# Performance work log

Measured on AMD Instinct MI355X. Metric: run time of the kernel, lower is better.

The kernel has to match this reference:

```python
import jax, jax.numpy as jnp
import numpy as np

EPS = 1e-5

def mean_std_norm(x):
    # instance norm without affine: per-(B,C) mean/std over spatial dims
    mean = jnp.mean(x, axis=(2, 3), keepdims=True)
    var = jnp.var(x, axis=(2, 3), keepdims=True)
    return (x - mean) / jnp.sqrt(var + EPS)

def conv1x1(x, w, b):
    # x: [B,C,H,W], w: [O,C], b: [O]
    return jnp.einsum('oc,bchw->bohw', w, x) + b[None, :, None, None]

def setup_inputs() -> dict:
    key = jax.random.key(0)
    ks = jax.random.split(key, 9)
    C = 512
    s = 1.0 / np.sqrt(C)
    inp = {
        'content_feat': jax.random.normal(ks[0], (4, C, 64, 64), dtype=jnp.float32),
        'f_w': jax.random.normal(ks[1], (C, C), dtype=jnp.float32) * s,
        'f_b': jnp.zeros((C,), dtype=jnp.float32),
        'g_w': jax.random.normal(ks[2], (C, C), dtype=jnp.float32) * s,
        'g_b': jnp.zeros((C,), dtype=jnp.float32),
        'h_w': jax.random.normal(ks[3], (C, C), dtype=jnp.float32) * s,
        'h_b': jnp.zeros((C,), dtype=jnp.float32),
        'o_w': jax.random.normal(ks[4], (C, C), dtype=jnp.float32) * s,
        'o_b': jnp.zeros((C,), dtype=jnp.float32),
    }
    return inp

def reference(content_feat, f_w, f_b, g_w, g_b, h_w, h_b, o_w, o_b):
    B, C, H, W = content_feat.shape
    HW = H * W
    norm = mean_std_norm(content_feat)
    # f(norm) -> [B, HW, C]; g(norm) -> [B, C, HW]
    F_Fc = conv1x1(norm, f_w, f_b).reshape(B, C, HW).transpose(0, 2, 1)
    G_Fs = conv1x1(norm, g_w, g_b).reshape(B, C, HW)
    energy = jnp.einsum('bnc,bcm->bnm', F_Fc, G_Fs)  # [B, HW, HW]
    attention = jax.nn.softmax(energy, axis=-1)
    H_Fs = conv1x1(content_feat, h_w, h_b).reshape(B, C, HW)
    # out = H_Fs @ attention^T : out[b,c,m] = sum_n H_Fs[b,c,n] * att[b,m,n]
    out = jnp.einsum('bcn,bmn->bcm', H_Fs, attention).reshape(B, C, H, W)
    out = conv1x1(out, o_w, o_b)
    return out + content_feat
```

## Files before the change

kernel.cpp:

```cpp
#include <hip/hip_runtime.h>


typedef __bf16 bf16_t;
typedef _Float16 f16_t;
typedef _Float16 f16x8 __attribute__((ext_vector_type(8)));
typedef float f32x4 __attribute__((ext_vector_type(4)));

#define LOG2E 1.44269504088896340736f

__device__ __forceinline__ void gload16(const void* g, void* l) {
  __builtin_amdgcn_global_load_lds(
      (const __attribute__((address_space(1))) void*)g,
      (__attribute__((address_space(3))) void*)l, 16, 0, 0);
}

__global__ void __launch_bounds__(256) stats_k(const float* __restrict__ x,
                                               float* __restrict__ mu,
                                               float* __restrict__ rs,
                                               f16_t* __restrict__ xv) {
  const int bc = blockIdx.x;
  const float4* row = (const float4*)(x + (size_t)bc * 4096);
  f16_t* vrow = xv + (size_t)bc * 4096;
  float s = 0.f, ss = 0.f;
  for (int i = threadIdx.x; i < 1024; i += 256) {
    float4 v = row[i];
    s += v.x + v.y + v.z + v.w;
    ss += v.x * v.x + v.y * v.y + v.z * v.z + v.w * v.w;
    alignas(8) f16_t h[4];
    h[0] = (f16_t)v.x; h[1] = (f16_t)v.y; h[2] = (f16_t)v.z; h[3] = (f16_t)v.w;
    *(uint2*)(vrow + i * 4) = *(const uint2*)h;
  }
#pragma unroll
  for (int o = 32; o >= 1; o >>= 1) {
    s += __shfl_down(s, o);
    ss += __shfl_down(ss, o);
  }
  __shared__ float as_[4], ass_[4];
  const int w = threadIdx.x >> 6;
  if ((threadIdx.x & 63) == 0) { as_[w] = s; ass_[w] = ss; }
  __syncthreads();
  if (threadIdx.x == 0) {
    float st = as_[0] + as_[1] + as_[2] + as_[3];
    float sst = ass_[0] + ass_[1] + ass_[2] + ass_[3];
    float m = st * (1.f / 4096.f);
    float var = sst * (1.f / 4096.f) - m * m;
    mu[bc] = m;
    rs[bc] = rsqrtf(var + 1e-5f);
  }
}

__device__ void mt_body(const float* __restrict__ A, const float* __restrict__ B,
                        f16_t* __restrict__ Out, int it, int jt, float* sm, bool bIsJK) {
  float* Fs = sm;
  float* Gs = sm + 2048;
  const int t = threadIdx.x;
  float acc[16];
#pragma unroll
  for (int i = 0; i < 16; ++i) acc[i] = 0.f;
  const int jl = t >> 2, ib = (t & 3) * 16;
  const int lr = t >> 4, lc4 = (t & 15) * 4;
  for (int cc = 0; cc < 16; ++cc) {
    __syncthreads();
#pragma unroll
    for (int rep = 0; rep < 2; ++rep) {
      const int r = lr + rep * 16;
      *(float4*)&Fs[r * 64 + lc4] = *(const float4*)(A + (size_t)(cc * 32 + r) * 512 + it * 64 + lc4);
      if (!bIsJK)
        *(float4*)&Gs[r * 64 + lc4] = *(const float4*)(B + (size_t)(cc * 32 + r) * 512 + jt * 64 + lc4);
    }
    if (bIsJK) {
      const int oj = t >> 2, ok = (t & 3) * 8;
      const float4 a = *(const float4*)(B + (size_t)(jt * 64 + oj) * 512 + cc * 32 + ok);
      const float4 bq = *(const float4*)(B + (size_t)(jt * 64 + oj) * 512 + cc * 32 + ok + 4);
      Gs[oj * 33 + ok] = a.x; Gs[oj * 33 + ok + 1] = a.y;
      Gs[oj * 33 + ok + 2] = a.z; Gs[oj * 33 + ok + 3] = a.w;
      Gs[oj * 33 + ok + 4] = bq.x; Gs[oj * 33 + ok + 5] = bq.y;
      Gs[oj * 33 + ok + 6] = bq.z; Gs[oj * 33 + ok + 7] = bq.w;
    }
    __syncthreads();
#pragma unroll
    for (int c = 0; c < 32; ++c) {
      const float gv = bIsJK ? Gs[jl * 33 + c] : Gs[c * 64 + jl];
#pragma unroll
      for (int ii = 0; ii < 16; ++ii) acc[ii] += gv * Fs[c * 64 + ib + ii];
    }
  }
  alignas(16) f16_t hi[16];
#pragma unroll
  for (int ii = 0; ii < 16; ++ii) hi[ii] = (f16_t)acc[ii];
  const size_t o = (size_t)(jt * 64 + jl) * 512 + it * 64 + ib;
  *(uint4*)(Out + o) = *(const uint4*)hi;
  *(uint4*)(Out + o + 8) = *(const uint4*)(hi + 8);
}

__global__ void __launch_bounds__(256) prep_k(const float* __restrict__ fw,
                                              const float* __restrict__ gw,
                                              const float* __restrict__ hw,
                                              const float* __restrict__ ow,
                                              const float* __restrict__ fb,
                                              const float* __restrict__ hb,
                                              const float* __restrict__ ob,
                                              f16_t* __restrict__ Mh,
                                              f16_t* __restrict__ Wf,
                                              float* __restrict__ vv,
                                              float* __restrict__ b2) {
  __shared__ float sm[2048 + 64 * 33];
  const int bb = blockIdx.x;
  if (bb < 64) {
    mt_body(fw, gw, Mh, bb & 7, bb >> 3, sm, false);
  } else if (bb < 128) {
    mt_body(hw, ow, Wf, (bb - 64) & 7, (bb - 64) >> 3, sm, true);
  } else if (bb < 130) {
    const int j = (bb - 128) * 256 + threadIdx.x;
    float s = 0.f;
    for (int c = 0; c < 512; ++c) s += gw[(size_t)c * 512 + j] * fb[c];
    vv[j] = s;
  } else {
    const int j = (bb - 130) * 256 + threadIdx.x;
    float s = 0.f;
    for (int c = 0; c < 512; ++c) s += ow[(size_t)j * 512 + c] * hb[c];
    b2[j] = s + ob[j];
  }
}

__global__ void __launch_bounds__(256) u_k(const float* __restrict__ v,
                                           const f16_t* __restrict__ xf,
                                           float* __restrict__ u) {
  const int w = threadIdx.x >> 6, lane = threadIdx.x & 63;
  const int m = blockIdx.x * 4 + w;
  const int b = blockIdx.y;
  const size_t o = ((size_t)b * 4096 + m) * 512 + lane * 8;
  const f16x8 vh = *(const f16x8*)(xf + o);
  const float4 v0 = *(const float4*)(v + lane * 8);
  const float4 v1 = *(const float4*)(v + lane * 8 + 4);
  float s = 0.f;
  const float* vp = &v0.x;
#pragma unroll
  for (int e = 0; e < 4; ++e) s += (float)vh[e] * vp[e];
  const float* vq = &v1.x;
#pragma unroll
  for (int e = 0; e < 4; ++e) s += (float)vh[4 + e] * vq[e];
#pragma unroll
  for (int o2 = 32; o2 >= 1; o2 >>= 1) s += __shfl_down(s, o2);
  if (lane == 0) u[(size_t)b * 4096 + m] = s;
}

__global__ void __launch_bounds__(256) normt_k(const float* __restrict__ x,
                                               const float* __restrict__ mu,
                                               const float* __restrict__ rs,
                                               f16_t* __restrict__ xf) {
  __shared__ float tile[64][65];
  const int t = threadIdx.x;
  const int nt = blockIdx.x, ct = blockIdx.y, b = blockIdx.z;
  const float* src = x + ((size_t)b * 512 + ct * 64) * 4096 + nt * 64;
  {
    const int r = t >> 4, cq = (t & 15) * 4;
#pragma unroll
    for (int it = 0; it < 4; ++it) {
      const int rr = r + it * 16;
      const float4 v = *(const float4*)(src + (size_t)rr * 4096 + cq);
      tile[rr][cq] = v.x; tile[rr][cq + 1] = v.y;
      tile[rr][cq + 2] = v.z; tile[rr][cq + 3] = v.w;
    }
  }
  __syncthreads();
  const int n = t & 63, ch = t >> 6;
  alignas(16) f16_t vf[16];
#pragma unroll
  for (int i = 0; i < 16; ++i) {
    const int c = ch * 16 + i;
    const float v = tile[c][n];
    const int gc = b * 512 + ct * 64 + c;
    vf[i] = (f16_t)((v - mu[gc]) * rs[gc]);
  }
  const size_t o = ((size_t)b * 4096 + nt * 64 + n) * 512 + ct * 64 + ch * 16;
  *(uint4*)(xf + o) = *(const uint4*)vf;
  *(uint4*)(xf + o + 8) = *(const uint4*)(vf + 8);
}

template <typename OT, int BIAS, bool RESID>
__global__ void __launch_bounds__(256) gemm_k(const f16_t* __restrict__ A,
                                              const f16_t* __restrict__ Bt,
                                              OT* __restrict__ C,
                                              const float* __restrict__ biasM,
                                              const float* __restrict__ biasN,
                                              const float* __restrict__ resid,
                                              long sAb, long sBb, long sCb, int ldC) {
  __shared__ alignas(16) f16_t As[2][128 * 64];
  __shared__ alignas(16) f16_t Bs[2][128 * 64];
  const int t = threadIdx.x;
  const int lane = t & 63;
  const int w = t >> 6;
  const int wr = w >> 1, wc = w & 1;
  const int l15 = lane & 15, lg = lane >> 4;
  const int b = blockIdx.z;
  const int m0 = blockIdx.y * 128, n0 = blockIdx.x * 128;
  const f16_t* Ab = A + (size_t)sAb * b + (size_t)m0 * 512;
  const f16_t* Bb = Bt + (size_t)sBb * b + (size_t)n0 * 512;
  const int srow = t >> 3;
  const int slot = t & 7;

  auto gstage = [&](int pb_, int ks_) {
#pragma unroll
    for (int r_ = 0; r_ < 4; ++r_) {
      const int rr_ = r_ * 32 + srow;
      const size_t go_ = (size_t)rr_ * 512 + ks_ * 64 + ((slot ^ (rr_ & 7)) * 8);
      gload16(Ab + go_, (char*)As[pb_] + r_ * 4096 + w * 1024);
      gload16(Bb + go_, (char*)Bs[pb_] + r_ * 4096 + w * 1024);
    }
  };

  const f32x4 z4 = {0.f, 0.f, 0.f, 0.f};
  f32x4 acc[4][4];
#pragma unroll
  for (int i = 0; i < 4; ++i)
#pragma unroll
    for (int j = 0; j < 4; ++j) acc[i][j] = z4;

  gstage(0, 0);
  __syncthreads();
  for (int ks = 0; ks < 8; ++ks) {
    const int pb = ks & 1;
    if (ks < 7) gstage(pb ^ 1, ks + 1);
#pragma unroll
    for (int kk = 0; kk < 2; ++kk) {
      f16x8 af[4], bfr[4];
#pragma unroll
      for (int i = 0; i < 4; ++i) {
        const int ra = wr * 64 + i * 16 + l15;
        af[i] = *(const f16x8*)((const char*)As[pb] + ra * 128 + (((kk * 4 + lg) ^ (ra & 7)) * 16));
        const int rb = wc * 64 + i * 16 + l15;
        bfr[i] = *(const f16x8*)((const char*)Bs[pb] + rb * 128 + (((kk * 4 + lg) ^ (rb & 7)) * 16));
      }
#pragma unroll
      for (int i = 0; i < 4; ++i)
#pragma unroll
        for (int j = 0; j < 4; ++j)
          acc[i][j] = __builtin_amdgcn_mfma_f32_16x16x32_f16(af[i], bfr[j], acc[i][j], 0, 0, 0);
    }
    __syncthreads();
  }
  OT* Cb = C + (size_t)sCb * b;
#pragma unroll
  for (int i = 0; i < 4; ++i) {
#pragma unroll
    for (int j = 0; j < 4; ++j) {
      const int n = n0 + wc * 64 + j * 16 + l15;
      float bn = 0.f;
      if (BIAS == 2) bn = biasN[n];
#pragma unroll
      for (int r = 0; r < 4; ++r) {
        const int m = m0 + wr * 64 + i * 16 + lg * 4 + r;
        float v = acc[i][j][r] + bn;
        if (BIAS == 1) v += biasM[m];
        if (RESID) v += resid[(size_t)sCb * b + (size_t)m * ldC + n];
        Cb[(size_t)m * ldC + n] = (OT)v;
      }
    }
  }
}

__global__ void __launch_bounds__(512, 1) flash_k(const f16_t* __restrict__ Z,
                                                  const f16_t* __restrict__ X,
                                                  const float* __restrict__ u,
                                                  const f16_t* __restrict__ Hv,
                                                  f16_t* __restrict__ Oat_t) {
  __shared__ alignas(16) f16_t K[2][64 * 256];
  __shared__ alignas(16) f16_t P[64 * 72];
  __shared__ float redm[4][2][16];
  __shared__ float reds[4][2][16];
  __shared__ float alds[64];
  __shared__ float llds[64];

  const int t = threadIdx.x;
  const int lane = t & 63;
  const int w = t >> 6;
  const int wq = w & 3, wk = w >> 2;
  const int l15 = lane & 15, lg = lane >> 4;
  const int bid = blockIdx.x;
  const int xcd = bid & 7;
  const int b = xcd >> 1;
  const int q0 = ((xcd & 1) * 32 + (bid >> 3)) * 64;

  const f16_t* Kb = X + (size_t)b * 4096 * 512;
  const f16_t* Vb = Hv + (size_t)b * 512 * 4096;
  const float* ub = u + (size_t)b * 4096;

  const int srow = w * 2 + (lane >> 5);
  const int slot32 = lane & 31;

  auto stagek = [&](int pb_, int kt_, int hf_) {
    const int k0_ = kt_ * 64;
#pragma unroll
    for (int r_ = 0; r_ < 4; ++r_) {
      const int row_ = r_ * 16 + srow;
      const size_t go_ = (size_t)(k0_ + row_) * 512 + hf_ * 256 + ((slot32 ^ (row_ & 7)) * 8);
      gload16(Kb + go_, (char*)K[pb_] + r_ * 8192 + w * 1024);
    }
  };

#define QKHALF(PB, HF)                                                                        \
  do {                                                                                        \
    _Pragma("unroll") for (int cwl_ = 0; cwl_ < 8; ++cwl_) {                                  \
      const f16x8 qf_ = qf[(HF) * 8 + cwl_];                                                  \
      _Pragma("unroll") for (int mf_ = 0; mf_ < 2; ++mf_) {                                   \
        const int key_ = 32 * wk + 16 * mf_ + l15;                                            \
        const int so_ = ((cwl_ * 4 + lg) ^ (key_ & 7)) * 16;                                  \
        const f16x8 kf_ = *(const f16x8*)((const char*)K[PB] + key_ * 512 + so_);             \
        sacc[mf_] = __builtin_amdgcn_mfma_f32_16x16x32_f16(kf_, qf_, sacc[mf_], 0, 0, 0);     \
      }                                                                                       \
    }                                                                                         \
  } while (0)

  f16x8 qf[16];
  {
    const size_t qo = ((size_t)b * 4096 + q0 + 16 * wq + l15) * 512 + lg * 8;
#pragma unroll
    for (int cw = 0; cw < 16; ++cw) qf[cw] = *(const f16x8*)(Z + qo + cw * 32);
  }
  stagek(0, 0, 0);

  const f32x4 z4 = {0.f, 0.f, 0.f, 0.f};
  f32x4 oacc[4][4];
#pragma unroll
  for (int i = 0; i < 4; ++i)
#pragma unroll
    for (int j = 0; j < 4; ++j) oacc[i][j] = z4;
  float m_run = -3.0e38f, l_run = 0.f;
  const int qrow = 16 * wq + l15;

  __syncthreads();

  for (int kt = 0; kt < 64; ++kt) {
    const int k0 = kt * 64;
    f32x4 sacc[2] = {z4, z4};
    const float4 u0 = *(const float4*)(ub + k0 + 32 * wk + 4 * lg);
    const float4 u1 = *(const float4*)(ub + k0 + 32 * wk + 16 + 4 * lg);
    stagek(1, kt, 1);
    QKHALF(0, 0);
    __syncthreads();
    if (kt < 63) stagek(0, kt + 1, 0);
    f16x8 vpre[4][2];
#pragma unroll
    for (int ct = 0; ct < 4; ++ct) {
      const int c = 64 * w + 16 * ct + l15;
#pragma unroll
      for (int kk = 0; kk < 2; ++kk)
        vpre[ct][kk] = *(const f16x8*)(Vb + (size_t)c * 4096 + k0 + kk * 32 + lg * 8);
    }
    QKHALF(1, 1);
    float pm = -3.0e38f;
    {
      const float* up0 = &u0.x;
      const float* up1 = &u1.x;
#pragma unroll
      for (int j = 0; j < 4; ++j) {
        sacc[0][j] += up0[j];
        sacc[1][j] += up1[j];
        pm = fmaxf(pm, fmaxf(sacc[0][j], sacc[1][j]));
      }
    }
    pm = fmaxf(pm, __shfl_xor(pm, 16));
    pm = fmaxf(pm, __shfl_xor(pm, 32));
    if (lane < 16) redm[wq][wk][lane] = pm;
    __syncthreads();
    const float m_tile = fmaxf(pm, redm[wq][wk ^ 1][l15]);
    float alpha;
    if (m_tile > m_run + 8.f) {
      alpha = exp2f((m_run - m_tile) * LOG2E);
      m_run = m_tile;
    } else {
      alpha = 1.f;
    }
    float ps = 0.f;
    {
      alignas(8) f16_t pk[4];
#pragma unroll
      for (int mf = 0; mf < 2; ++mf) {
#pragma unroll
        for (int j = 0; j < 4; ++j) {
          const float p = exp2f((sacc[mf][j] - m_run) * LOG2E);
          ps += p;
          pk[j] = (f16_t)p;
        }
        *(uint2*)((char*)P + qrow * 144 + 64 * wk + 32 * mf + 8 * lg) = *(const uint2*)pk;
      }
    }
    ps += __shfl_xor(ps, 16);
    ps += __shfl_xor(ps, 32);
    if (lane < 16) {
      reds[wq][wk][lane] = ps;
      if (wk == 0) alds[16 * wq + lane] = alpha;
    }
    __syncthreads();
    const float s_tile = reds[wq][0][l15] + reds[wq][1][l15];
    l_run = l_run * alpha + s_tile;
    float aq[4];
#pragma unroll
    for (int qt = 0; qt < 4; ++qt) aq[qt] = alds[16 * qt + l15];
    const bool need = (aq[0] != 1.f) || (aq[1] != 1.f) || (aq[2] != 1.f) || (aq[3] != 1.f);
    if (__any(need)) {
#pragma unroll
      for (int ct = 0; ct < 4; ++ct)
#pragma unroll
        for (int qt = 0; qt < 4; ++qt) oacc[ct][qt] *= aq[qt];
    }
#pragma unroll
    for (int kk = 0; kk < 2; ++kk) {
      f16x8 bp[4];
#pragma unroll
      for (int qt = 0; qt < 4; ++qt) {
        const int q = 16 * qt + l15;
        bp[qt] = *(const f16x8*)((const char*)P + q * 144 + kk * 64 + lg * 16);
      }
#pragma unroll
      for (int ct = 0; ct < 4; ++ct)
#pragma unroll
        for (int qt = 0; qt < 4; ++qt)
          oacc[ct][qt] =
              __builtin_amdgcn_mfma_f32_16x16x32_f16(vpre[ct][kk], bp[qt], oacc[ct][qt], 0, 0, 0);
    }
  }
#undef QKHALF
  if (wk == 0 && lane < 16) llds[16 * wq + lane] = l_run;
  __syncthreads();
  float inv[4];
#pragma unroll
  for (int qt = 0; qt < 4; ++qt) inv[qt] = 1.f / llds[16 * qt + l15];
#pragma unroll
  for (int ct = 0; ct < 4; ++ct)
#pragma unroll
    for (int qt = 0; qt < 4; ++qt) {
      alignas(8) f16_t o4[4];
#pragma unroll
      for (int j = 0; j < 4; ++j) o4[j] = (f16_t)(oacc[ct][qt][j] * inv[qt]);
      *(uint2*)(Oat_t + ((size_t)b * 4096 + q0 + 16 * qt + l15) * 512 + 64 * w + 16 * ct + 4 * lg) =
          *(const uint2*)o4;
    }
}

extern "C" void kernel_launch(void* const* d_in, const int* in_sizes, int n_in,
                              void* d_out, int out_size, void* d_ws, size_t ws_size,
                              hipStream_t stream) {
  const float* x = (const float*)d_in[0];
  const float* fw = (const float*)d_in[1];
  const float* fb = (const float*)d_in[2];
  const float* gw = (const float*)d_in[3];
  const float* gb = (const float*)d_in[4];
  const float* hw = (const float*)d_in[5];
  const float* hb = (const float*)d_in[6];
  const float* ow = (const float*)d_in[7];
  const float* ob = (const float*)d_in[8];
  float* out = (float*)d_out;
  (void)gb;

  const size_t BIG = (size_t)4 * 4096 * 512 * sizeof(f16_t);
  char* p = (char*)d_ws;
  float* mu = (float*)p; p += 2048 * sizeof(float);
  float* rs = (float*)p; p += 2048 * sizeof(float);
  float* vv = (float*)p; p += 512 * sizeof(float);
  float* b2 = (float*)p; p += 512 * sizeof(float);
  float* uu = (float*)p; p += (size_t)4 * 4096 * sizeof(float);
  f16_t* Mh = (f16_t*)p; p += (size_t)512 * 512 * sizeof(f16_t);
  f16_t* Wf = (f16_t*)p; p += (size_t)512 * 512 * sizeof(f16_t);
  f16_t* xf = (f16_t*)p; p += BIG;
  f16_t* xv = (f16_t*)p; p += BIG;
  f16_t* Zf = (f16_t*)p; p += BIG;
  f16_t* Oat_t = (f16_t*)p; p += BIG;

  const long sD = (long)4096 * 512;

  stats_k<<<2048, 256, 0, stream>>>(x, mu, rs, xv);
  prep_k<<<132, 256, 0, stream>>>(fw, gw, hw, ow, fb, hb, ob, Mh, Wf, vv, b2);
  normt_k<<<dim3(64, 8, 4), 256, 0, stream>>>(x, mu, rs, xf);
  u_k<<<dim3(1024, 4), 256, 0, stream>>>(vv, xf, uu);
  gemm_k<f16_t, 0, false><<<dim3(4, 32, 4), 256, 0, stream>>>(
      xf, Mh, Zf, nullptr, nullptr, nullptr, sD, 0, sD, 512);
  flash_k<<<256, 512, 0, stream>>>(Zf, xf, uu, xv, Oat_t);
  gemm_k<float, 1, true><<<dim3(32, 4, 4), 256, 0, stream>>>(
      Wf, Oat_t, out, b2, nullptr, x, 0, sD, sD, 4096);

  (void)in_sizes; (void)n_in; (void)out_size; (void)ws_size;
}
```

Measured before the change: 364.9 us.

## Fuse Z projection GEMM into flash attention prologue via LDS

Removes the separate gemm_k launch that computed Z = xf·Mh into a global buffer. Each flash block now computes its own 64-query slice of Z with MFMAs, reading Mh and xf directly from global memory, and keeps the result in a new padded LDS array that the query fragments are loaded from. This drops one kernel launch and a full write and read of the Z tensor. In exchange the prologue adds unstaged global loads and a serial GEMM phase before the attention loop, and the larger LDS footprint could limit occupancy.

```diff
diff --git a/kernel.cpp b/kernel.cpp
--- a/kernel.cpp
+++ b/kernel.cpp
@@ -260,13 +260,14 @@
   }
 }
 
-__global__ void __launch_bounds__(512, 1) flash_k(const f16_t* __restrict__ Z,
+__global__ void __launch_bounds__(512, 1) flash_k(const f16_t* __restrict__ Mh,
                                                   const f16_t* __restrict__ X,
                                                   const float* __restrict__ u,
                                                   const f16_t* __restrict__ Hv,
                                                   f16_t* __restrict__ Oat_t) {
   __shared__ alignas(16) f16_t K[2][64 * 256];
   __shared__ alignas(16) f16_t P[64 * 72];
+  __shared__ alignas(16) f16_t Zl[64 * 528];
   __shared__ float redm[4][2][16];
   __shared__ float reds[4][2][16];
   __shared__ float alds[64];
@@ -285,6 +286,41 @@
   const f16_t* Kb = X + (size_t)b * 4096 * 512;
   const f16_t* Vb = Hv + (size_t)b * 512 * 4096;
   const float* ub = u + (size_t)b * 4096;
+
+  const f32x4 z4 = {0.f, 0.f, 0.f, 0.f};
+
+  {
+    f32x4 zacc[4][4];
+#pragma unroll
+    for (int qs = 0; qs < 4; ++qs)
+#pragma unroll
+      for (int jtl = 0; jtl < 4; ++jtl) zacc[qs][jtl] = z4;
+    for (int kw = 0; kw < 16; ++kw) {
+      f16x8 Af[4], Bf[4];
+#pragma unroll
+      for (int jtl = 0; jtl < 4; ++jtl)
+        Af[jtl] = *(const f16x8*)(Mh + (size_t)((w * 4 + jtl) * 16 + l15) * 512 + kw * 32 + lg * 8);
+#pragma unroll
+      for (int qs = 0; qs < 4; ++qs)
+        Bf[qs] = *(const f16x8*)(Kb + (size_t)(q0 + qs * 16 + l15) * 512 + kw * 32 + lg * 8);
+#pragma unroll
+      for (int qs = 0; qs < 4; ++qs)
+#pragma unroll
+        for (int jtl = 0; jtl < 4; ++jtl)
+          zacc[qs][jtl] = __builtin_amdgcn_mfma_f32_16x16x32_f16(Af[jtl], Bf[qs], zacc[qs][jtl], 0, 0, 0);
+    }
+#pragma unroll
+    for (int qs = 0; qs < 4; ++qs)
+#pragma unroll
+      for (int jtl = 0; jtl < 4; ++jtl) {
+        alignas(8) f16_t zk[4];
+#pragma unroll
+        for (int r = 0; r < 4; ++r) zk[r] = (f16_t)zacc[qs][jtl][r];
+        *(uint2*)((char*)Zl + (16 * qs + l15) * 1056 + ((w * 4 + jtl) * 16 + lg * 4) * 2) =
+            *(const uint2*)zk;
+      }
+  }
+  __syncthreads();
 
   const int srow = w * 2 + (lane >> 5);
   const int slot32 = lane & 31;
@@ -312,15 +348,12 @@
     }                                                                                         \
   } while (0)
 
+  stagek(0, 0, 0);
   f16x8 qf[16];
-  {
-    const size_t qo = ((size_t)b * 4096 + q0 + 16 * wq + l15) * 512 + lg * 8;
-#pragma unroll
-    for (int cw = 0; cw < 16; ++cw) qf[cw] = *(const f16x8*)(Z + qo + cw * 32);
-  }
-  stagek(0, 0, 0);
-
-  const f32x4 z4 = {0.f, 0.f, 0.f, 0.f};
+#pragma unroll
+  for (int cw = 0; cw < 16; ++cw)
+    qf[cw] = *(const f16x8*)((const char*)Zl + (16 * wq + l15) * 1056 + (cw * 32 + lg * 8) * 2);
+
   f32x4 oacc[4][4];
 #pragma unroll
   for (int i = 0; i < 4; ++i)
@@ -465,7 +498,6 @@
   f16_t* Wf = (f16_t*)p; p += (size_t)512 * 512 * sizeof(f16_t);
   f16_t* xf = (f16_t*)p; p += BIG;
   f16_t* xv = (f16_t*)p; p += BIG;
-  f16_t* Zf = (f16_t*)p; p += BIG;
   f16_t* Oat_t = (f16_t*)p; p += BIG;
 
   const long sD = (long)4096 * 512;
@@ -474,9 +506,7 @@
   prep_k<<<132, 256, 0, stream>>>(fw, gw, hw, ow, fb, hb, ob, Mh, Wf, vv, b2);
   normt_k<<<dim3(64, 8, 4), 256, 0, stream>>>(x, mu, rs, xf);
   u_k<<<dim3(1024, 4), 256, 0, stream>>>(vv, xf, uu);
-  gemm_k<f16_t, 0, false><<<dim3(4, 32, 4), 256, 0, stream>>>(
-      xf, Mh, Zf, nullptr, nullptr, nullptr, sD, 0, sD, 512);
-  flash_k<<<256, 512, 0, stream>>>(Zf, xf, uu, xv, Oat_t);
+  flash_k<<<256, 512, 0, stream>>>(Mh, xf, uu, xv, Oat_t);
   gemm_k<float, 1, true><<<dim3(32, 4, 4), 256, 0, stream>>>(
       Wf, Oat_t, out, b2, nullptr, x, 0, sD, sD, 4096);
 
```

Result: slower. 373.0 us (+2.2%).
